# Kernel optimization log

Hardware: AMD Instinct MI355X
Metric: run time of the kernel (lower is better)

The kernel has to match this reference:

```python
import jax, jax.numpy as jnp
import numpy as np

ETA = 1e-5
MIN_SIGMA = 1e-6

def setup_inputs() -> dict:
    key = jax.random.key(0)
    k1, k2, k3, k4 = jax.random.split(key, 4)
    B, N0, N1, D = 32, 1024, 1024, 128
    xt = jax.random.normal(k1, (B, D), dtype=jnp.float32)
    t = jax.random.uniform(k2, (B,), dtype=jnp.float32)
    x0_ref = jax.random.normal(k3, (N0, D), dtype=jnp.float32)
    x1_ref = jax.random.normal(k4, (N1, D), dtype=jnp.float32)
    sigma_w = jnp.zeros((1,), dtype=jnp.float32)  # learned scalar of the sigma_model
    return {"xt": xt, "t": t, "x0_ref": x0_ref, "x1_ref": x1_ref, "sigma_w": sigma_w}


def reference(xt, t, x0_ref, x1_ref, sigma_w):
    # Equivalent to ExplicitFlowMatcher.compute_explicit_flow_vcond (implementation='vcond',
    # use_full_gaussian_prefactor=True). The chunked online-softmax loop computes exactly a
    # softmax over all (N0,N1) pairs; here we express it with GEMMs instead of materializing
    # the [B,N0,N1,D] conditional-flow tensor (v_cond is affine in x0, x1, xt so the weighted
    # sum decomposes into matmuls).
    B, D = xt.shape
    Df = jnp.asarray(D, xt.dtype)

    # pairwise squared distances ||x1_j - x0_i||^2 via norms + GEMM  -> [N0,N1]
    x0n = jnp.sum(x0_ref * x0_ref, axis=-1)            # [N0]
    x1n = jnp.sum(x1_ref * x1_ref, axis=-1)            # [N1]
    dot01 = x0_ref @ x1_ref.T                          # [N0,N1]
    dist01 = x0n[:, None] + x1n[None, :] - 2.0 * dot01  # [N0,N1]

    # sigma_model: softplus(w)*||x1-x0||/sqrt(D) + min_sigma, then bridge scale in t
    sigma_space = jax.nn.softplus(sigma_w[0]) * jnp.sqrt(jnp.maximum(dist01, 0.0) / Df) + MIN_SIGMA
    bridge = jnp.sqrt((t + ETA) * (1.0 - t + ETA))     # [B]
    sigma_t = sigma_space[None, :, :] * bridge[:, None, None]  # [B,N0,N1]

    # ||xt_b - mu_t(i,j)||^2 with mu_t = (1-t)x0 + t x1, expanded into GEMM terms
    tb = t[:, None, None]
    omt = 1.0 - tb
    xtn = jnp.sum(xt * xt, axis=-1)                    # [B]
    xt_x0 = xt @ x0_ref.T                              # [B,N0]
    xt_x1 = xt @ x1_ref.T                              # [B,N1]
    mu_norm2 = (omt * omt) * x0n[None, :, None] + (tb * tb) * x1n[None, None, :] \
               + (2.0 * tb * omt) * dot01[None, :, :]
    xt_mu = omt * xt_x0[:, :, None] + tb * xt_x1[:, None, :]
    dist2 = xtn[:, None, None] - 2.0 * xt_mu + mu_norm2  # [B,N0,N1]

    # Gaussian log-weight with full prefactor
    logw = -dist2 / (2.0 * sigma_t * sigma_t) - Df * jnp.log(sigma_t)  # [B,N0,N1]

    # stable softmax over the (N0,N1) pairs (== the online max/den/num recursion)
    m = jnp.max(logw, axis=(1, 2), keepdims=True)
    w = jnp.exp(logw - m)                               # [B,N0,N1]
    den = jnp.sum(w, axis=(1, 2))                       # [B]

    # v_cond = x1 - x0 + c_t*(xt - mu_t) = c_t*xt + a*x0 + b*x1 (affine in x0,x1)
    c_t = (1.0 - 2.0 * t) / (2.0 * (t + ETA) * (1.0 - t + ETA))  # [B]
    a = -1.0 - c_t * (1.0 - t)
    b = 1.0 - c_t * t
    wx0 = jnp.einsum('bij,id->bd', w, x0_ref)
    wx1 = jnp.einsum('bij,jd->bd', w, x1_ref)

    den_c = jnp.maximum(den, 1e-12)[:, None]
    num = c_t[:, None] * xt * den[:, None] + a[:, None] * wx0 + b[:, None] * wx1
    return num / den_c
```

## Files before the change

### kernel.cpp

```cpp
#include <hip/hip_runtime.h>
#include <math.h>

#define ETA 1e-5f
#define MIN_SIGMA 1e-6f

constexpr int NN = 1024;
constexpr int ND = 128;

constexpr size_t OFF_MAXKEY = 0;
constexpr size_t OFF_DEN    = 32;
constexpr size_t OFF_RW     = 64;
constexpr size_t OFF_CW     = OFF_RW + 32 * 1024;
constexpr size_t OFF_X0N    = OFF_CW + 32 * 1024;
constexpr size_t OFF_X1N    = OFF_X0N + 1024;
constexpr size_t OFF_AP     = OFF_X1N + 1024;
constexpr size_t OFF_BP     = OFF_AP + 32 * 1024;
constexpr size_t OFF_C2     = OFF_BP + 32 * 1024;
constexpr size_t OFF_RWP    = ((OFF_C2 + 32 + 63) / 64) * 64;
constexpr size_t OFF_DOT    = OFF_RWP;
constexpr size_t OFF_CWP    = OFF_RWP + 32 * 32 * 1024;
constexpr size_t OFF_MLOC   = OFF_CWP + 32 * 32 * 1024;
constexpr size_t WS_NEED_FUSED = OFF_MLOC + 32 * 32 * 32;
constexpr size_t WS_NEED_FALLBACK = OFF_DOT + 1024 * 1024;

__device__ __forceinline__ unsigned fkey(float x) {
  unsigned u = __float_as_uint(x);
  return (u & 0x80000000u) ? ~u : (u | 0x80000000u);
}
__device__ __forceinline__ float funkey(unsigned u) {
  return (u & 0x80000000u) ? __uint_as_float(u & 0x7fffffffu)
                           : __uint_as_float(~u);
}

__global__ __launch_bounds__(256) void k_ab(const float* __restrict__ xt,
                                            const float* __restrict__ tarr,
                                            const float* __restrict__ x0,
                                            const float* __restrict__ x1,
                                            float* __restrict__ ws) {
  __shared__ __align__(16) float xts[ND];
  int b = blockIdx.x >> 2, q = blockIdx.x & 3;
  int tid = threadIdx.x;
  if (tid < ND) xts[tid] = xt[(size_t)b * ND + tid];
  __syncthreads();

  float tb = tarr[b];
  float omt = 1.f - tb;
  float ib2 = 1.f / ((tb + ETA) * (1.f - tb + ETA));

  float xtn = 0.f;
#pragma unroll
  for (int k4 = 0; k4 < ND / 4; k4++) {
    float4 xv = *(const float4*)&xts[k4 * 4];
    xtn += xv.x * xv.x + xv.y * xv.y + xv.z * xv.z + xv.w * xv.w;
  }

  int i = q * 256 + tid;
  float acc0 = 0.f, acc1 = 0.f, n0 = 0.f, n1 = 0.f;
#pragma unroll 8
  for (int k4 = 0; k4 < ND / 4; k4++) {
    float4 xv = *(const float4*)&xts[k4 * 4];
    float4 a = *(const float4*)(x0 + (size_t)i * ND + k4 * 4);
    float4 c = *(const float4*)(x1 + (size_t)i * ND + k4 * 4);
    acc0 += xv.x * a.x + xv.y * a.y + xv.z * a.z + xv.w * a.w;
    acc1 += xv.x * c.x + xv.y * c.y + xv.z * c.z + xv.w * c.w;
    n0 += a.x * a.x + a.y * a.y + a.z * a.z + a.w * a.w;
    n1 += c.x * c.x + c.y * c.y + c.z * c.z + c.w * c.w;
  }
  ws[OFF_AP + (size_t)b * NN + i] =
      fmaf(omt * omt, n0, fmaf(-2.f * omt, acc0, xtn)) * ib2;
  ws[OFF_BP + (size_t)b * NN + i] =
      fmaf(tb * tb, n1, -2.f * tb * acc1) * ib2;
  if (b == 0) {
    ws[OFF_X0N + i] = n0;
    ws[OFF_X1N + i] = n1;
  }
  if (q == 0 && tid == 0) ws[OFF_C2 + b] = 2.f * tb * omt * ib2;
}

__global__ __launch_bounds__(256) void kF(const float* __restrict__ x0,
                                          const float* __restrict__ x1,
                                          const float* __restrict__ sigw,
                                          float* __restrict__ ws) {
  __shared__ __align__(16) float gemmbuf[2304];
  __shared__ __align__(16) float4 QPRS[32][32];
  __shared__ float ApT[32][33], BpT[32][33];
  __shared__ float x0nS[32], x1nS[32];
  __shared__ unsigned mS[32];

  float (*As)[36] = (float(*)[36])&gemmbuf[0];
  float (*Bs)[36] = (float(*)[36])&gemmbuf[1152];
  float (*rowP)[33] = (float(*)[33])&gemmbuf[0];
  float (*colS)[33] = (float(*)[33])&gemmbuf[1056];

  int tid = threadIdx.x;
  int tx = tid & 15, ty = tid >> 4;
  int jb = blockIdx.x, ib = blockIdx.y;
  int i0 = ib * 32, j0 = jb * 32;

  {
    const float* Ap = ws + OFF_AP;
    const float* Bp = ws + OFF_BP;
#pragma unroll
    for (int rep = 0; rep < 4; rep++) {
      int idx = rep * 256 + tid;
      int bb = idx >> 5, ii = idx & 31;
      ApT[ii][bb] = Ap[(size_t)bb * NN + i0 + ii];
      BpT[ii][bb] = Bp[(size_t)bb * NN + j0 + ii];
    }
    if (tid < 32) {
      x0nS[tid] = ws[OFF_X0N + i0 + tid];
      x1nS[tid] = ws[OFF_X1N + j0 + tid];
      mS[tid] = 0u;
    }
  }

  float c00 = 0.f, c01 = 0.f, c10 = 0.f, c11 = 0.f;
  int srow = tid >> 3, sk4 = tid & 7;
  for (int kc = 0; kc < 4; kc++) {
    __syncthreads();
    float4 a = *(const float4*)(x0 + (size_t)(i0 + srow) * ND + kc * 32 + sk4 * 4);
    float4 bb = *(const float4*)(x1 + (size_t)(j0 + srow) * ND + kc * 32 + sk4 * 4);
    As[sk4 * 4 + 0][srow] = a.x;
    As[sk4 * 4 + 1][srow] = a.y;
    As[sk4 * 4 + 2][srow] = a.z;
    As[sk4 * 4 + 3][srow] = a.w;
    Bs[sk4 * 4 + 0][srow] = bb.x;
    Bs[sk4 * 4 + 1][srow] = bb.y;
    Bs[sk4 * 4 + 2][srow] = bb.z;
    Bs[sk4 * 4 + 3][srow] = bb.w;
    __syncthreads();
#pragma unroll
    for (int k = 0; k < 32; k++) {
      float2 av = *(const float2*)&As[k][ty * 2];
      float2 bv = *(const float2*)&Bs[k][tx * 2];
      c00 = fmaf(av.x, bv.x, c00);
      c01 = fmaf(av.x, bv.y, c01);
      c10 = fmaf(av.y, bv.x, c10);
      c11 = fmaf(av.y, bv.y, c11);
    }
  }

  float swv = sigw[0];
  float sp = (swv > 20.f) ? swv : log1pf(__expf(swv));
  float dotv[2][2] = {{c00, c01}, {c10, c11}};
#pragma unroll
  for (int r = 0; r < 2; r++) {
#pragma unroll
    for (int c = 0; c < 2; c++) {
      float d01 = x0nS[ty * 2 + r] + x1nS[tx * 2 + c] - 2.f * dotv[r][c];
      float ss = fmaf(sp, sqrtf(fmaxf(d01, 0.f) * (1.f / 128.f)), MIN_SIGMA);
      float Q = -0.72134752044f / (ss * ss);
      float R = -128.f * __log2f(ss);
      QPRS[ty * 2 + r][tx * 2 + c] = make_float4(Q, dotv[r][c] * Q, R, 0.f);
    }
  }
  __syncthreads();

  for (int idx = tid; idx < 1056; idx += 256) ((float*)rowP)[idx] = 0.f;
  int b = tid & 31, jg = tid >> 5;
  float c2b = ws[OFF_C2 + b];
  float bp4[4];
#pragma unroll
  for (int jj = 0; jj < 4; jj++) bp4[jj] = BpT[jg * 4 + jj][b];
  float m = -3.4e38f;
#pragma unroll
  for (int i = 0; i < 32; i++) {
    float ap = ApT[i][b];
#pragma unroll
    for (int jj = 0; jj < 4; jj++) {
      float4 q4 = QPRS[i][jg * 4 + jj];
      float core = fmaf(ap + bp4[jj], q4.x, fmaf(c2b, q4.y, q4.z));
      m = fmaxf(m, core);
    }
  }
  atomicMax(&mS[b], fkey(m));
  __syncthreads();

  float m2 = funkey(mS[b]);
  float col4[4] = {0.f, 0.f, 0.f, 0.f};
#pragma unroll
  for (int i = 0; i < 32; i++) {
    float ap = ApT[i][b];
    float rs = 0.f;
#pragma unroll
    for (int jj = 0; jj < 4; jj++) {
      float4 q4 = QPRS[i][jg * 4 + jj];
      float core = fmaf(ap + bp4[jj], q4.x, fmaf(c2b, q4.y, q4.z));
      float w = exp2f(core - m2);
      rs += w;
      col4[jj] += w;
    }
    atomicAdd(&rowP[i][b], rs);
  }
#pragma unroll
  for (int jj = 0; jj < 4; jj++) colS[jg * 4 + jj][b] = col4[jj];
  __syncthreads();

  float* rwp = ws + OFF_RWP + (size_t)jb * (32 * 1024);
  float* cwp = ws + OFF_CWP + (size_t)ib * (32 * 1024);
#pragma unroll
  for (int k = 0; k < 4; k++) {
    int idx = k * 256 + tid;
    int bb = idx >> 5, ii = idx & 31;
    rwp[(size_t)bb * NN + i0 + ii] = rowP[ii][bb];
    cwp[(size_t)bb * NN + j0 + ii] = colS[ii][bb];
  }
  if (tid < 32) ws[OFF_MLOC + ((size_t)ib * 32 + jb) * 32 + tid] = funkey(mS[tid]);
}

__global__ __launch_bounds__(256) void kR(float* __restrict__ ws) {
  __shared__ float red[256];
  int b = blockIdx.x >> 2, quarter = blockIdx.x & 3;
  int tid = threadIdx.x;

  const float* ml = ws + OFF_MLOC + b;
  float mx = -3.4e38f;
#pragma unroll
  for (int k = 0; k < 4; k++) mx = fmaxf(mx, ml[(size_t)(k * 256 + tid) * 32]);
  red[tid] = mx;
  __syncthreads();
  for (int s = 128; s > 0; s >>= 1) {
    if (tid < s) red[tid] = fmaxf(red[tid], red[tid + s]);
    __syncthreads();
  }
  float mg = red[0];
  __syncthreads();

  int i = quarter * 256 + tid;
  int tb = i >> 5;
  const float* rwp = ws + OFF_RWP + (size_t)b * NN + i;
  const float* cwp = ws + OFF_CWP + (size_t)b * NN + i;
  const float* mlI = ws + OFF_MLOC + (size_t)tb * 1024 + b;
  const float* mlJ = ws + OFF_MLOC + (size_t)tb * 32 + b;
  float s0 = 0.f, s1 = 0.f;
#pragma unroll 8
  for (int p = 0; p < 32; p++) {
    s0 = fmaf(exp2f(mlI[(size_t)p * 32] - mg), rwp[(size_t)p * 32 * 1024], s0);
    s1 = fmaf(exp2f(mlJ[(size_t)p * 1024] - mg), cwp[(size_t)p * 32 * 1024], s1);
  }
  ws[OFF_RW + (size_t)b * NN + i] = s0;
  ws[OFF_CW + (size_t)b * NN + i] = s1;

  red[tid] = s0;
  __syncthreads();
  for (int s = 128; s > 0; s >>= 1) {
    if (tid < s) red[tid] += red[tid + s];
    __syncthreads();
  }
  if (tid == 0) atomicAdd(ws + OFF_DEN + b, red[0]);
}

__global__ __launch_bounds__(256) void k1(const float* __restrict__ x0,
                                          const float* __restrict__ x1,
                                          const float* __restrict__ sigw,
                                          float* __restrict__ ws) {
  __shared__ __align__(16) float As[32][36];
  __shared__ __align__(16) float Bs[32][36];
  __shared__ __align__(16) float4 QPRS[32][32];
  __shared__ float ApT[32][33], BpT[32][33];
  __shared__ float x0nS[32], x1nS[32];
  __shared__ unsigned mS[32];

  int tid = threadIdx.x;
  int tx = tid & 15, ty = tid >> 4;
  int i0 = blockIdx.y * 32, j0 = blockIdx.x * 32;

  {
    const float* Ap = ws + OFF_AP;
    const float* Bp = ws + OFF_BP;
#pragma unroll
    for (int rep = 0; rep < 4; rep++) {
      int idx = rep * 256 + tid;
      int bb = idx >> 5, ii = idx & 31;
      ApT[ii][bb] = Ap[(size_t)bb * NN + i0 + ii];
      BpT[ii][bb] = Bp[(size_t)bb * NN + j0 + ii];
    }
    if (tid < 32) {
      x0nS[tid] = ws[OFF_X0N + i0 + tid];
      x1nS[tid] = ws[OFF_X1N + j0 + tid];
      mS[tid] = 0u;
    }
  }

  float c00 = 0.f, c01 = 0.f, c10 = 0.f, c11 = 0.f;
  int srow = tid >> 3, sk4 = tid & 7;
  for (int kc = 0; kc < 4; kc++) {
    __syncthreads();
    float4 a = *(const float4*)(x0 + (size_t)(i0 + srow) * ND + kc * 32 + sk4 * 4);
    float4 bb = *(const float4*)(x1 + (size_t)(j0 + srow) * ND + kc * 32 + sk4 * 4);
    As[sk4 * 4 + 0][srow] = a.x;
    As[sk4 * 4 + 1][srow] = a.y;
    As[sk4 * 4 + 2][srow] = a.z;
    As[sk4 * 4 + 3][srow] = a.w;
    Bs[sk4 * 4 + 0][srow] = bb.x;
    Bs[sk4 * 4 + 1][srow] = bb.y;
    Bs[sk4 * 4 + 2][srow] = bb.z;
    Bs[sk4 * 4 + 3][srow] = bb.w;
    __syncthreads();
#pragma unroll
    for (int k = 0; k < 32; k++) {
      float2 av = *(const float2*)&As[k][ty * 2];
      float2 bv = *(const float2*)&Bs[k][tx * 2];
      c00 = fmaf(av.x, bv.x, c00);
      c01 = fmaf(av.x, bv.y, c01);
      c10 = fmaf(av.y, bv.x, c10);
      c11 = fmaf(av.y, bv.y, c11);
    }
  }

  float* dot = ws + OFF_DOT;
  *(float2*)&dot[(size_t)(i0 + ty * 2 + 0) * NN + j0 + tx * 2] = make_float2(c00, c01);
  *(float2*)&dot[(size_t)(i0 + ty * 2 + 1) * NN + j0 + tx * 2] = make_float2(c10, c11);

  float swv = sigw[0];
  float sp = (swv > 20.f) ? swv : log1pf(__expf(swv));
  float dotv[2][2] = {{c00, c01}, {c10, c11}};
#pragma unroll
  for (int r = 0; r < 2; r++) {
#pragma unroll
    for (int c = 0; c < 2; c++) {
      float d01 = x0nS[ty * 2 + r] + x1nS[tx * 2 + c] - 2.f * dotv[r][c];
      float ss = fmaf(sp, sqrtf(fmaxf(d01, 0.f) * (1.f / 128.f)), MIN_SIGMA);
      float Q = -0.72134752044f / (ss * ss);
      float R = -128.f * __log2f(ss);
      QPRS[ty * 2 + r][tx * 2 + c] = make_float4(Q, dotv[r][c] * Q, R, 0.f);
    }
  }
  __syncthreads();

  int b = tid & 31, rep = tid >> 5;
  float c2b = ws[OFF_C2 + b];
  float bpreg[32];
#pragma unroll
  for (int j = 0; j < 32; j++) bpreg[j] = BpT[j][b];
  float m = -3.4e38f;
#pragma unroll
  for (int r = 0; r < 4; r++) {
    int i = rep * 4 + r;
    float ap = ApT[i][b];
#pragma unroll
    for (int j = 0; j < 32; j++) {
      float4 q4 = QPRS[i][j];
      float core = fmaf(ap + bpreg[j], q4.x, fmaf(c2b, q4.y, q4.z));
      m = fmaxf(m, core);
    }
  }
  atomicMax(&mS[b], fkey(m));
  __syncthreads();
  if (tid < 32) atomicMax((unsigned*)ws + OFF_MAXKEY + tid, mS[tid]);
}

__global__ __launch_bounds__(256) void k2(const float* __restrict__ sigw,
                                          float* __restrict__ ws) {
  __shared__ __align__(16) float4 QPRS[32][32];
  __shared__ float ApT[32][33], BpT[32][33];
  __shared__ float colS[32][33], rowS[32][33];
  __shared__ float x0nS[32], x1nS[32];
  __shared__ float denS[32];

  int tid = threadIdx.x;
  int tx = tid & 15, ty = tid >> 4;
  int i0 = blockIdx.y * 32, j0 = blockIdx.x * 32;

  {
    const float* Ap = ws + OFF_AP;
    const float* Bp = ws + OFF_BP;
#pragma unroll
    for (int rep = 0; rep < 4; rep++) {
      int idx = rep * 256 + tid;
      int bb = idx >> 5, ii = idx & 31;
      ApT[ii][bb] = Ap[(size_t)bb * NN + i0 + ii];
      BpT[ii][bb] = Bp[(size_t)bb * NN + j0 + ii];
      colS[ii][bb] = 0.f;
    }
    if (tid < 32) {
      x0nS[tid] = ws[OFF_X0N + i0 + tid];
      x1nS[tid] = ws[OFF_X1N + j0 + tid];
      denS[tid] = 0.f;
    }
  }

  const float* dot = ws + OFF_DOT;
  float2 dv0 = *(const float2*)&dot[(size_t)(i0 + ty * 2 + 0) * NN + j0 + tx * 2];
  float2 dv1 = *(const float2*)&dot[(size_t)(i0 + ty * 2 + 1) * NN + j0 + tx * 2];
  float dotv[2][2] = {{dv0.x, dv0.y}, {dv1.x, dv1.y}};
  float swv = sigw[0];
  float sp = (swv > 20.f) ? swv : log1pf(__expf(swv));

  __syncthreads();

#pragma unroll
  for (int r = 0; r < 2; r++) {
#pragma unroll
    for (int c = 0; c < 2; c++) {
      float d01 = x0nS[ty * 2 + r] + x1nS[tx * 2 + c] - 2.f * dotv[r][c];
      float ss = fmaf(sp, sqrtf(fmaxf(d01, 0.f) * (1.f / 128.f)), MIN_SIGMA);
      float Q = -0.72134752044f / (ss * ss);
      float R = -128.f * __log2f(ss);
      QPRS[ty * 2 + r][tx * 2 + c] = make_float4(Q, dotv[r][c] * Q, R, 0.f);
    }
  }
  __syncthreads();

  int b = tid & 31, rep = tid >> 5;
  float c2b = ws[OFF_C2 + b];
  float m2 = funkey(((const unsigned*)ws)[OFF_MAXKEY + b]);
  float bpreg[32];
#pragma unroll
  for (int j = 0; j < 32; j++) bpreg[j] = BpT[j][b];
  float colreg[32];
#pragma unroll
  for (int j = 0; j < 32; j++) colreg[j] = 0.f;
  float dreg = 0.f;
#pragma unroll
  for (int r = 0; r < 4; r++) {
    int i = rep * 4 + r;
    float ap = ApT[i][b];
    float rs = 0.f;
#pragma unroll
    for (int j = 0; j < 32; j++) {
      float4 q4 = QPRS[i][j];
      float core = fmaf(ap + bpreg[j], q4.x, fmaf(c2b, q4.y, q4.z));
      float w = exp2f(core - m2);
      rs += w;
      colreg[j] += w;
    }
    rowS[i][b] = rs;
    dreg += rs;
  }
#pragma unroll
  for (int j = 0; j < 32; j++) atomicAdd(&colS[j][b], colreg[j]);
  atomicAdd(&denS[b], dreg);
  __syncthreads();

  float* rw = ws + OFF_RW;
  float* cw = ws + OFF_CW;
#pragma unroll
  for (int k = 0; k < 4; k++) {
    int idx = k * 256 + tid;
    int bb = idx >> 5, ii = idx & 31;
    atomicAdd(&rw[(size_t)bb * NN + i0 + ii], rowS[ii][bb]);
    atomicAdd(&cw[(size_t)bb * NN + j0 + ii], colS[ii][bb]);
  }
  if (tid < 32) atomicAdd(ws + OFF_DEN + tid, denS[tid]);
}

__global__ __launch_bounds__(256) void k3(const float* __restrict__ xt,
                                          const float* __restrict__ tarr,
                                          const float* __restrict__ x0,
                                          const float* __restrict__ x1,
                                          const float* __restrict__ ws,
                                          float* __restrict__ out) {
  int b = blockIdx.x >> 2, dq = blockIdx.x & 3;
  int tid = threadIdx.x;
  int d = dq * 32 + (tid & 31);
  int h = tid >> 5;
  const float* rw = ws + OFF_RW + (size_t)b * NN;
  const float* cw = ws + OFF_CW + (size_t)b * NN;
  float a0 = 0.f, a1 = 0.f;
  int ibeg = h * 128;
#pragma unroll 4
  for (int k = 0; k < 128; k++) {
    int i = ibeg + k;
    a0 = fmaf(rw[i], x0[(size_t)i * ND + d], a0);
    a1 = fmaf(cw[i], x1[(size_t)i * ND + d], a1);
  }
  __shared__ float s0[8][32], s1[8][32];
  s0[h][tid & 31] = a0;
  s1[h][tid & 31] = a1;
  __syncthreads();
  if (tid < 32) {
    float A0 = 0.f, A1 = 0.f;
#pragma unroll
    for (int hh = 0; hh < 8; hh++) {
      A0 += s0[hh][tid];
      A1 += s1[hh][tid];
    }
    float tb = tarr[b];
    float den = ws[OFF_DEN + b];
    float ct = (1.f - 2.f * tb) / (2.f * (tb + ETA) * (1.f - tb + ETA));
    float av = -1.f - ct * (1.f - tb);
    float bv = 1.f - ct * tb;
    float den_c = fmaxf(den, 1e-12f);
    out[(size_t)b * ND + d] =
        (ct * xt[(size_t)b * ND + d] * den + av * A0 + bv * A1) / den_c;
  }
}

extern "C" void kernel_launch(void* const* d_in, const int* in_sizes, int n_in,
                              void* d_out, int out_size, void* d_ws, size_t ws_size,
                              hipStream_t stream) {
  const float* xt = (const float*)d_in[0];
  const float* t = (const float*)d_in[1];
  const float* x0 = (const float*)d_in[2];
  const float* x1 = (const float*)d_in[3];
  const float* sw = (const float*)d_in[4];
  float* out = (float*)d_out;
  float* ws = (float*)d_ws;

  bool fused = ws_size >= WS_NEED_FUSED * sizeof(float);

  if (fused) {
    hipMemsetAsync(ws, 0, 64 * sizeof(float), stream);
    k_ab<<<128, 256, 0, stream>>>(xt, t, x0, x1, ws);
    kF<<<dim3(32, 32), 256, 0, stream>>>(x0, x1, sw, ws);
    kR<<<128, 256, 0, stream>>>(ws);
  } else {
    hipMemsetAsync(ws, 0, OFF_X0N * sizeof(float), stream);
    k_ab<<<128, 256, 0, stream>>>(xt, t, x0, x1, ws);
    k1<<<dim3(32, 32), 256, 0, stream>>>(x0, x1, sw, ws);
    k2<<<dim3(32, 32), 256, 0, stream>>>(sw, ws);
  }
  k3<<<32 * 4, 256, 0, stream>>>(xt, t, x0, x1, ws, out);
}
```

Baseline: 161.8 us.

## Split fused pair kernel into GEMM and batch-parallel softmax passes, widen grids

The fused pair kernel is split in two. kG computes the x0·x1 GEMM and writes per-pair Q, P, R coefficients to global memory. kE then handles the per-batch max and exp-sum over a 3D grid with batches split into groups of eight, raising block-level parallelism. k_ab now uses eight threads per row with shuffle reductions, and k3 uses more blocks with a tree reduction, so each grid has many more blocks. The cost is three extra 4 MB global arrays written and read four times each, plus shared-memory atomicAdd on column sums in the inner loop.

```diff
diff --git a/kernel.cpp b/kernel.cpp
--- a/kernel.cpp
+++ b/kernel.cpp
@@ -16,11 +16,14 @@
 constexpr size_t OFF_AP     = OFF_X1N + 1024;
 constexpr size_t OFF_BP     = OFF_AP + 32 * 1024;
 constexpr size_t OFF_C2     = OFF_BP + 32 * 1024;
-constexpr size_t OFF_RWP    = ((OFF_C2 + 32 + 63) / 64) * 64;
-constexpr size_t OFF_DOT    = OFF_RWP;
+constexpr size_t OFF_QA     = ((OFF_C2 + 32 + 255) / 256) * 256;
+constexpr size_t OFF_DOT    = OFF_QA;
+constexpr size_t OFF_PA     = OFF_QA + 1024 * 1024;
+constexpr size_t OFF_RA     = OFF_PA + 1024 * 1024;
+constexpr size_t OFF_RWP    = OFF_RA + 1024 * 1024;
 constexpr size_t OFF_CWP    = OFF_RWP + 32 * 32 * 1024;
 constexpr size_t OFF_MLOC   = OFF_CWP + 32 * 32 * 1024;
-constexpr size_t WS_NEED_FUSED = OFF_MLOC + 32 * 32 * 32;
+constexpr size_t WS_NEED_NEW = OFF_MLOC + 32 * 32 * 32;
 constexpr size_t WS_NEED_FALLBACK = OFF_DOT + 1024 * 1024;
 
 __device__ __forceinline__ unsigned fkey(float x) {
@@ -38,7 +41,7 @@
                                             const float* __restrict__ x1,
                                             float* __restrict__ ws) {
   __shared__ __align__(16) float xts[ND];
-  int b = blockIdx.x >> 2, q = blockIdx.x & 3;
+  int b = blockIdx.x >> 5, strip = blockIdx.x & 31;
   int tid = threadIdx.x;
   if (tid < ND) xts[tid] = xt[(size_t)b * ND + tid];
   __syncthreads();
@@ -47,71 +50,59 @@
   float omt = 1.f - tb;
   float ib2 = 1.f / ((tb + ETA) * (1.f - tb + ETA));
 
-  float xtn = 0.f;
-#pragma unroll
-  for (int k4 = 0; k4 < ND / 4; k4++) {
-    float4 xv = *(const float4*)&xts[k4 * 4];
-    xtn += xv.x * xv.x + xv.y * xv.y + xv.z * xv.z + xv.w * xv.w;
-  }
-
-  int i = q * 256 + tid;
-  float acc0 = 0.f, acc1 = 0.f, n0 = 0.f, n1 = 0.f;
-#pragma unroll 8
-  for (int k4 = 0; k4 < ND / 4; k4++) {
-    float4 xv = *(const float4*)&xts[k4 * 4];
-    float4 a = *(const float4*)(x0 + (size_t)i * ND + k4 * 4);
-    float4 c = *(const float4*)(x1 + (size_t)i * ND + k4 * 4);
+  int r = strip * 32 + (tid >> 3);
+  int q8 = tid & 7;
+  const float* xr = &xts[q8 * 16];
+  const float* a0p = x0 + (size_t)r * ND + q8 * 16;
+  const float* a1p = x1 + (size_t)r * ND + q8 * 16;
+  float acc0 = 0.f, acc1 = 0.f, n0 = 0.f, n1 = 0.f, xtn = 0.f;
+#pragma unroll
+  for (int k4 = 0; k4 < 4; k4++) {
+    float4 xv = *(const float4*)&xr[k4 * 4];
+    float4 a = *(const float4*)&a0p[k4 * 4];
+    float4 c = *(const float4*)&a1p[k4 * 4];
     acc0 += xv.x * a.x + xv.y * a.y + xv.z * a.z + xv.w * a.w;
     acc1 += xv.x * c.x + xv.y * c.y + xv.z * c.z + xv.w * c.w;
     n0 += a.x * a.x + a.y * a.y + a.z * a.z + a.w * a.w;
     n1 += c.x * c.x + c.y * c.y + c.z * c.z + c.w * c.w;
-  }
-  ws[OFF_AP + (size_t)b * NN + i] =
-      fmaf(omt * omt, n0, fmaf(-2.f * omt, acc0, xtn)) * ib2;
-  ws[OFF_BP + (size_t)b * NN + i] =
-      fmaf(tb * tb, n1, -2.f * tb * acc1) * ib2;
-  if (b == 0) {
-    ws[OFF_X0N + i] = n0;
-    ws[OFF_X1N + i] = n1;
-  }
-  if (q == 0 && tid == 0) ws[OFF_C2 + b] = 2.f * tb * omt * ib2;
-}
-
-__global__ __launch_bounds__(256) void kF(const float* __restrict__ x0,
+    xtn += xv.x * xv.x + xv.y * xv.y + xv.z * xv.z + xv.w * xv.w;
+  }
+#pragma unroll
+  for (int off = 1; off < 8; off <<= 1) {
+    acc0 += __shfl_xor(acc0, off, 64);
+    acc1 += __shfl_xor(acc1, off, 64);
+    n0 += __shfl_xor(n0, off, 64);
+    n1 += __shfl_xor(n1, off, 64);
+    xtn += __shfl_xor(xtn, off, 64);
+  }
+  if (q8 == 0) {
+    ws[OFF_AP + (size_t)b * NN + r] =
+        fmaf(omt * omt, n0, fmaf(-2.f * omt, acc0, xtn)) * ib2;
+    ws[OFF_BP + (size_t)b * NN + r] =
+        fmaf(tb * tb, n1, -2.f * tb * acc1) * ib2;
+    if (b == 0) {
+      ws[OFF_X0N + r] = n0;
+      ws[OFF_X1N + r] = n1;
+    }
+  }
+  if (strip == 0 && tid == 0) ws[OFF_C2 + b] = 2.f * tb * omt * ib2;
+}
+
+__global__ __launch_bounds__(256) void kG(const float* __restrict__ x0,
                                           const float* __restrict__ x1,
                                           const float* __restrict__ sigw,
                                           float* __restrict__ ws) {
-  __shared__ __align__(16) float gemmbuf[2304];
-  __shared__ __align__(16) float4 QPRS[32][32];
-  __shared__ float ApT[32][33], BpT[32][33];
+  __shared__ __align__(16) float As[32][36];
+  __shared__ __align__(16) float Bs[32][36];
   __shared__ float x0nS[32], x1nS[32];
-  __shared__ unsigned mS[32];
-
-  float (*As)[36] = (float(*)[36])&gemmbuf[0];
-  float (*Bs)[36] = (float(*)[36])&gemmbuf[1152];
-  float (*rowP)[33] = (float(*)[33])&gemmbuf[0];
-  float (*colS)[33] = (float(*)[33])&gemmbuf[1056];
 
   int tid = threadIdx.x;
   int tx = tid & 15, ty = tid >> 4;
-  int jb = blockIdx.x, ib = blockIdx.y;
-  int i0 = ib * 32, j0 = jb * 32;
-
-  {
-    const float* Ap = ws + OFF_AP;
-    const float* Bp = ws + OFF_BP;
-#pragma unroll
-    for (int rep = 0; rep < 4; rep++) {
-      int idx = rep * 256 + tid;
-      int bb = idx >> 5, ii = idx & 31;
-      ApT[ii][bb] = Ap[(size_t)bb * NN + i0 + ii];
-      BpT[ii][bb] = Bp[(size_t)bb * NN + j0 + ii];
-    }
-    if (tid < 32) {
-      x0nS[tid] = ws[OFF_X0N + i0 + tid];
-      x1nS[tid] = ws[OFF_X1N + j0 + tid];
-      mS[tid] = 0u;
-    }
+  int i0 = blockIdx.y * 32, j0 = blockIdx.x * 32;
+
+  if (tid < 32) {
+    x0nS[tid] = ws[OFF_X0N + i0 + tid];
+    x1nS[tid] = ws[OFF_X1N + j0 + tid];
   }
 
   float c00 = 0.f, c01 = 0.f, c10 = 0.f, c11 = 0.f;
@@ -143,69 +134,92 @@
   float swv = sigw[0];
   float sp = (swv > 20.f) ? swv : log1pf(__expf(swv));
   float dotv[2][2] = {{c00, c01}, {c10, c11}};
+  float* QA = ws + OFF_QA;
+  float* PA = ws + OFF_PA;
+  float* RA = ws + OFF_RA;
 #pragma unroll
   for (int r = 0; r < 2; r++) {
+    float q2[2], p2[2], r2[2];
 #pragma unroll
     for (int c = 0; c < 2; c++) {
       float d01 = x0nS[ty * 2 + r] + x1nS[tx * 2 + c] - 2.f * dotv[r][c];
       float ss = fmaf(sp, sqrtf(fmaxf(d01, 0.f) * (1.f / 128.f)), MIN_SIGMA);
       float Q = -0.72134752044f / (ss * ss);
-      float R = -128.f * __log2f(ss);
-      QPRS[ty * 2 + r][tx * 2 + c] = make_float4(Q, dotv[r][c] * Q, R, 0.f);
-    }
-  }
-  __syncthreads();
-
-  for (int idx = tid; idx < 1056; idx += 256) ((float*)rowP)[idx] = 0.f;
-  int b = tid & 31, jg = tid >> 5;
+      q2[c] = Q;
+      p2[c] = dotv[r][c] * Q;
+      r2[c] = -128.f * __log2f(ss);
+    }
+    size_t g = (size_t)(i0 + ty * 2 + r) * NN + j0 + tx * 2;
+    *(float2*)&QA[g] = make_float2(q2[0], q2[1]);
+    *(float2*)&PA[g] = make_float2(p2[0], p2[1]);
+    *(float2*)&RA[g] = make_float2(r2[0], r2[1]);
+  }
+}
+
+__global__ __launch_bounds__(256) void kE(float* __restrict__ ws) {
+  __shared__ __align__(16) float QS[32][33], PS[32][33], RS[32][33];
+  __shared__ float BpS[32][9], colS[32][9];
+  __shared__ unsigned mS[8];
+
+  int tid = threadIdx.x;
+  int jb = blockIdx.x, ib = blockIdx.y, bq = blockIdx.z;
+  int i0 = ib * 32, j0 = jb * 32;
+  int i = tid & 31, b8 = tid >> 5;
+  int b = bq * 8 + b8;
+
+  {
+    const float* QA = ws + OFF_QA;
+    const float* PA = ws + OFF_PA;
+    const float* RA = ws + OFF_RA;
+#pragma unroll
+    for (int rep = 0; rep < 4; rep++) {
+      int idx = rep * 256 + tid;
+      int r = idx >> 5, c = idx & 31;
+      size_t g = (size_t)(i0 + r) * NN + j0 + c;
+      QS[r][c] = QA[g];
+      PS[r][c] = PA[g];
+      RS[r][c] = RA[g];
+    }
+  }
+  {
+    int j = tid & 31, bb = tid >> 5;
+    BpS[j][bb] = ws[OFF_BP + (size_t)(bq * 8 + bb) * NN + j0 + j];
+    colS[j][bb] = 0.f;
+  }
+  if (tid < 8) mS[tid] = 0u;
+  float ap = ws[OFF_AP + (size_t)b * NN + i0 + i];
   float c2b = ws[OFF_C2 + b];
-  float bp4[4];
-#pragma unroll
-  for (int jj = 0; jj < 4; jj++) bp4[jj] = BpT[jg * 4 + jj][b];
+  __syncthreads();
+
   float m = -3.4e38f;
 #pragma unroll
-  for (int i = 0; i < 32; i++) {
-    float ap = ApT[i][b];
-#pragma unroll
-    for (int jj = 0; jj < 4; jj++) {
-      float4 q4 = QPRS[i][jg * 4 + jj];
-      float core = fmaf(ap + bp4[jj], q4.x, fmaf(c2b, q4.y, q4.z));
-      m = fmaxf(m, core);
-    }
-  }
-  atomicMax(&mS[b], fkey(m));
-  __syncthreads();
-
-  float m2 = funkey(mS[b]);
-  float col4[4] = {0.f, 0.f, 0.f, 0.f};
-#pragma unroll
-  for (int i = 0; i < 32; i++) {
-    float ap = ApT[i][b];
-    float rs = 0.f;
-#pragma unroll
-    for (int jj = 0; jj < 4; jj++) {
-      float4 q4 = QPRS[i][jg * 4 + jj];
-      float core = fmaf(ap + bp4[jj], q4.x, fmaf(c2b, q4.y, q4.z));
-      float w = exp2f(core - m2);
-      rs += w;
-      col4[jj] += w;
-    }
-    atomicAdd(&rowP[i][b], rs);
-  }
-#pragma unroll
-  for (int jj = 0; jj < 4; jj++) colS[jg * 4 + jj][b] = col4[jj];
-  __syncthreads();
-
-  float* rwp = ws + OFF_RWP + (size_t)jb * (32 * 1024);
-  float* cwp = ws + OFF_CWP + (size_t)ib * (32 * 1024);
-#pragma unroll
-  for (int k = 0; k < 4; k++) {
-    int idx = k * 256 + tid;
-    int bb = idx >> 5, ii = idx & 31;
-    rwp[(size_t)bb * NN + i0 + ii] = rowP[ii][bb];
-    cwp[(size_t)bb * NN + j0 + ii] = colS[ii][bb];
-  }
-  if (tid < 32) ws[OFF_MLOC + ((size_t)ib * 32 + jb) * 32 + tid] = funkey(mS[tid]);
+  for (int jj = 0; jj < 32; jj++) {
+    int j = (jj + i) & 31;
+    float core = fmaf(ap + BpS[j][b8], QS[i][j], fmaf(c2b, PS[i][j], RS[i][j]));
+    m = fmaxf(m, core);
+  }
+  atomicMax(&mS[b8], fkey(m));
+  __syncthreads();
+  float m2 = funkey(mS[b8]);
+
+  float rs = 0.f;
+#pragma unroll
+  for (int jj = 0; jj < 32; jj++) {
+    int j = (jj + i) & 31;
+    float core = fmaf(ap + BpS[j][b8], QS[i][j], fmaf(c2b, PS[i][j], RS[i][j]));
+    float w = exp2f(core - m2);
+    rs += w;
+    atomicAdd(&colS[j][b8], w);
+  }
+  ws[OFF_RWP + (size_t)jb * (32 * 1024) + (size_t)b * NN + i0 + i] = rs;
+  __syncthreads();
+  {
+    int j = tid & 31, bb = tid >> 5;
+    ws[OFF_CWP + (size_t)ib * (32 * 1024) + (size_t)(bq * 8 + bb) * NN + j0 + j] =
+        colS[j][bb];
+  }
+  if (tid < 8)
+    ws[OFF_MLOC + ((size_t)ib * 32 + jb) * 32 + bq * 8 + tid] = funkey(mS[tid]);
 }
 
 __global__ __launch_bounds__(256) void kR(float* __restrict__ ws) {
@@ -451,31 +465,31 @@
                                           const float* __restrict__ x1,
                                           const float* __restrict__ ws,
                                           float* __restrict__ out) {
-  int b = blockIdx.x >> 2, dq = blockIdx.x & 3;
-  int tid = threadIdx.x;
-  int d = dq * 32 + (tid & 31);
-  int h = tid >> 5;
+  __shared__ float s0[32][8], s1[32][8];
+  int b = blockIdx.x >> 4, strip = blockIdx.x & 15;
+  int tid = threadIdx.x;
+  int c = tid & 7, h = tid >> 3;
+  int d = strip * 8 + c;
   const float* rw = ws + OFF_RW + (size_t)b * NN;
   const float* cw = ws + OFF_CW + (size_t)b * NN;
   float a0 = 0.f, a1 = 0.f;
-  int ibeg = h * 128;
 #pragma unroll 4
-  for (int k = 0; k < 128; k++) {
-    int i = ibeg + k;
+  for (int k = 0; k < 32; k++) {
+    int i = h * 32 + k;
     a0 = fmaf(rw[i], x0[(size_t)i * ND + d], a0);
     a1 = fmaf(cw[i], x1[(size_t)i * ND + d], a1);
   }
-  __shared__ float s0[8][32], s1[8][32];
-  s0[h][tid & 31] = a0;
-  s1[h][tid & 31] = a1;
-  __syncthreads();
-  if (tid < 32) {
-    float A0 = 0.f, A1 = 0.f;
-#pragma unroll
-    for (int hh = 0; hh < 8; hh++) {
-      A0 += s0[hh][tid];
-      A1 += s1[hh][tid];
-    }
+  s0[h][c] = a0;
+  s1[h][c] = a1;
+  __syncthreads();
+  for (int s = 16; s > 0; s >>= 1) {
+    if (h < s) {
+      s0[h][c] += s0[h + s][c];
+      s1[h][c] += s1[h + s][c];
+    }
+    __syncthreads();
+  }
+  if (h == 0) {
     float tb = tarr[b];
     float den = ws[OFF_DEN + b];
     float ct = (1.f - 2.f * tb) / (2.f * (tb + ETA) * (1.f - tb + ETA));
@@ -483,7 +497,7 @@
     float bv = 1.f - ct * tb;
     float den_c = fmaxf(den, 1e-12f);
     out[(size_t)b * ND + d] =
-        (ct * xt[(size_t)b * ND + d] * den + av * A0 + bv * A1) / den_c;
+        (ct * xt[(size_t)b * ND + d] * den + av * s0[0][c] + bv * s1[0][c]) / den_c;
   }
 }
 
@@ -498,18 +512,19 @@
   float* out = (float*)d_out;
   float* ws = (float*)d_ws;
 
-  bool fused = ws_size >= WS_NEED_FUSED * sizeof(float);
-
-  if (fused) {
+  bool newpath = ws_size >= WS_NEED_NEW * sizeof(float);
+
+  if (newpath) {
     hipMemsetAsync(ws, 0, 64 * sizeof(float), stream);
-    k_ab<<<128, 256, 0, stream>>>(xt, t, x0, x1, ws);
-    kF<<<dim3(32, 32), 256, 0, stream>>>(x0, x1, sw, ws);
+    k_ab<<<1024, 256, 0, stream>>>(xt, t, x0, x1, ws);
+    kG<<<dim3(32, 32), 256, 0, stream>>>(x0, x1, sw, ws);
+    kE<<<dim3(32, 32, 4), 256, 0, stream>>>(ws);
     kR<<<128, 256, 0, stream>>>(ws);
   } else {
     hipMemsetAsync(ws, 0, OFF_X0N * sizeof(float), stream);
-    k_ab<<<128, 256, 0, stream>>>(xt, t, x0, x1, ws);
+    k_ab<<<1024, 256, 0, stream>>>(xt, t, x0, x1, ws);
     k1<<<dim3(32, 32), 256, 0, stream>>>(x0, x1, sw, ws);
     k2<<<dim3(32, 32), 256, 0, stream>>>(sw, ws);
   }
-  k3<<<32 * 4, 256, 0, stream>>>(xt, t, x0, x1, ws, out);
-}
+  k3<<<512, 256, 0, stream>>>(xt, t, x0, x1, ws, out);
+}
```

Result: slower. 300.3 us (+85.6%).
